# Kernel optimization log

Hardware: AMD Instinct MI355X
Metric: run time of the kernel (lower is better)

Reference implementation:

```python
import jax, jax.numpy as jnp
from jax import lax
import numpy as np

IN, HID, NCLS, B, S = 360, 64, 5, 64, 128
MH_CONST = 2.0 / (np.sqrt(3.0) * np.pi ** 0.25)


def setup_inputs() -> dict:
    key = jax.random.key(0)
    ks = jax.random.split(key, 24)
    g = lambda i, shape, s=0.05: jax.random.normal(ks[i], shape, jnp.float32) * s
    inp = {
        'x_seq': jax.random.normal(ks[0], (B, S, IN), jnp.float32),
        # WavKANLinear params (out=64, in=360)
        'wav_scale': jnp.ones((HID, IN), jnp.float32),
        'wav_translation': jnp.zeros((HID, IN), jnp.float32),
        'wav_weights': g(1, (HID, IN)),
        'base_weight': g(2, (HID, IN)),
        # BatchNorm1d (eval mode, running stats)
        'bn_gamma': jnp.ones((HID,), jnp.float32),
        'bn_beta': jnp.zeros((HID,), jnp.float32),
        'bn_mean': jnp.zeros((HID,), jnp.float32),
        'bn_var': jnp.ones((HID,), jnp.float32),
        # LayerNorm(64)
        'ln_gamma': jnp.ones((HID,), jnp.float32),
        'ln_beta': jnp.zeros((HID,), jnp.float32),
        # bidirectional GRU, 1 layer, hidden=64
        'gru_w_ih_f': g(3, (3 * HID, HID)), 'gru_w_hh_f': g(4, (3 * HID, HID)),
        'gru_b_ih_f': g(5, (3 * HID,)), 'gru_b_hh_f': g(6, (3 * HID,)),
        'gru_w_ih_b': g(7, (3 * HID, HID)), 'gru_w_hh_b': g(8, (3 * HID, HID)),
        'gru_b_ih_b': g(9, (3 * HID,)), 'gru_b_hh_b': g(10, (3 * HID,)),
        # classifier: Linear(128,64) -> ReLU -> Linear(64,5)
        'fc1_w': g(11, (HID, 2 * HID)), 'fc1_b': jnp.zeros((HID,), jnp.float32),
        'fc2_w': g(12, (NCLS, HID)), 'fc2_b': jnp.zeros((NCLS,), jnp.float32),
    }
    return inp


def _gru_dir(x_sbf, w_ih, w_hh, b_ih, b_hh, reverse):
    # x_sbf: (S, B, F). Returns final hidden (B, H). PyTorch GRU equations.
    Bn = x_sbf.shape[1]
    H = w_hh.shape[1]
    gi_all = jnp.einsum('sbf,gf->sbg', x_sbf, w_ih) + b_ih  # precompute input gates

    def step(h, gi):
        gh = h @ w_hh.T + b_hh
        i_r, i_z, i_n = jnp.split(gi, 3, axis=-1)
        h_r, h_z, h_n = jnp.split(gh, 3, axis=-1)
        r = jax.nn.sigmoid(i_r + h_r)
        z = jax.nn.sigmoid(i_z + h_z)
        n = jnp.tanh(i_n + r * h_n)
        h_new = (1.0 - z) * n + z * h
        return h_new, None

    h0 = jnp.zeros((Bn, H), x_sbf.dtype)
    h_final, _ = lax.scan(step, h0, gi_all, reverse=reverse)
    return h_final


def reference(x_seq, wav_scale, wav_translation, wav_weights, base_weight,
              bn_gamma, bn_beta, bn_mean, bn_var, ln_gamma, ln_beta,
              gru_w_ih_f, gru_w_hh_f, gru_b_ih_f, gru_b_hh_f,
              gru_w_ih_b, gru_w_hh_b, gru_b_ih_b, gru_b_hh_b,
              fc1_w, fc1_b, fc2_w, fc2_b):
    b, s, f = x_seq.shape
    x_flat = x_seq.reshape(b * s, f)  # (N, 360)

    # --- WavKANLinear (mexican_hat) ---
    x_scaled = (x_flat[:, None, :] - wav_translation[None]) / wav_scale[None]  # (N, 64, 360)
    wavelet = MH_CONST * (x_scaled * x_scaled - 1.0) * jnp.exp(-0.5 * x_scaled * x_scaled)
    wav_out = jnp.einsum('noi,oi->no', wavelet, wav_weights)  # (N, 64)
    base_out = jax.nn.silu(x_flat) @ base_weight.T
    combined = wav_out + base_out
    # BatchNorm1d eval mode
    x_emb = (combined - bn_mean) * lax.rsqrt(bn_var + 1e-5) * bn_gamma + bn_beta

    # --- LayerNorm(64) ---
    mu = jnp.mean(x_emb, axis=-1, keepdims=True)
    var = jnp.mean(jnp.square(x_emb - mu), axis=-1, keepdims=True)
    x_emb = (x_emb - mu) * lax.rsqrt(var + 1e-5) * ln_gamma + ln_beta
    # dropout is identity in eval mode

    x_sbf = x_emb.reshape(b, s, HID).swapaxes(0, 1)  # (S, B, 64)

    # --- bidirectional GRU, take final hiddens ---
    h_fwd = _gru_dir(x_sbf, gru_w_ih_f, gru_w_hh_f, gru_b_ih_f, gru_b_hh_f, False)
    h_bwd = _gru_dir(x_sbf, gru_w_ih_b, gru_w_hh_b, gru_b_ih_b, gru_b_hh_b, True)
    hidden_cat = jnp.concatenate([h_fwd, h_bwd], axis=1)  # (B, 128)

    # --- classifier ---
    h = jax.nn.relu(hidden_cat @ fc1_w.T + fc1_b)
    logits = h @ fc2_w.T + fc2_b
    return logits
```

## Files before the change

kernel.cpp:

```cpp
#include <hip/hip_runtime.h>

#define IN_F   360
#define HIDN   64
#define NCLS   5
#define BATCH  64
#define SEQ    128
#define NROWS  (BATCH*SEQ)

#define WS_FLAG  0
#define WS_WPACK 16
#define WS_WFAST 92176
#define WS_WT4   138256
#define WS_XEMB  162832
#define WS_GI    687120
#define WS_HC    3832848

#define LOG2E        1.4426950408889634f
#define NEG_HALF_L2E (-0.7213475204444817f)

__device__ __forceinline__ float fast_rcp(float x) { return __builtin_amdgcn_rcpf(x); }
__device__ __forceinline__ float fast_rsq(float x) { return __builtin_amdgcn_rsqf(x); }
__device__ __forceinline__ float sigmoid_(float x) {
    x = fminf(fmaxf(x, -60.0f), 60.0f);
    return fast_rcp(1.0f + exp2f(-LOG2E * x));
}
__device__ __forceinline__ float tanh_(float x) {
    x = fminf(fmaxf(x, -30.0f), 30.0f);
    float e = exp2f(-2.8853900817779268f * x);
    return (1.0f - e) * fast_rcp(1.0f + e);
}
__device__ __forceinline__ float readlane_f(float v, int l) {
    return __int_as_float(__builtin_amdgcn_readlane(__float_as_int(v), l));
}

__global__ __launch_bounds__(256) void prep_kernel(
    const float* __restrict__ scale, const float* __restrict__ trans,
    const float* __restrict__ ww,    const float* __restrict__ bw,
    const float* __restrict__ wihf,  const float* __restrict__ wihb,
    float* __restrict__ ws) {
    int idx = blockIdx.x * 256 + threadIdx.x;
    float4* wpack  = (float4*)(ws + WS_WPACK);
    float2* wfast2 = (float2*)(ws + WS_WFAST);
    float*  wT4    = ws + WS_WT4;
    int*    flagp  = (int*)(ws + WS_FLAG);
    if (idx < 64 * IN_F) {
        int o = idx & 63, i = idx >> 6;
        float s  = scale[o * IN_F + i];
        float tr = trans[o * IN_F + i];
        if (s != 1.0f || tr != 0.0f) atomicOr(flagp, 1);
        float a  = 1.0f / s;
        float b  = -tr * a;
        float wq = 0.8673250705840776f * ww[o * IN_F + i];
        float bb = bw[o * IN_F + i];
        wpack[i * 64 + o] = make_float4(a, b, wq, bb);
        wfast2[(i >> 1) * 128 + o * 2 + (i & 1)] = make_float2(wq, bb);
    }
    int idx2 = idx - 64 * IN_F;
    if (idx2 >= 0 && idx2 < 24576) {
        int e = idx2 & 3; int rest = idx2 >> 2;
        int g = rest % 384; int k4 = rest / 384;
        int k = k4 * 4 + e; int dir = g / 192; int gg = g - dir * 192;
        const float* src = dir ? wihb : wihf;
        wT4[idx2] = src[gg * 64 + k];
    }
}

__global__ __launch_bounds__(256) void wavkan_kernel(
    const float* __restrict__ x_seq,
    const float* __restrict__ bn_g, const float* __restrict__ bn_b,
    const float* __restrict__ bn_m, const float* __restrict__ bn_v,
    const float* __restrict__ ln_g, const float* __restrict__ ln_b,
    const float* __restrict__ ws_c, float* __restrict__ x_emb) {
    __shared__ float2 xs_lds[16 * IN_F];
    int t = threadIdx.x;
    int row0 = blockIdx.x * 16;
    int o = t & 63, grp = t >> 6;
    int fast = (*(const int*)(ws_c + WS_FLAG)) == 0;

    float acc0 = 0.f, acc1 = 0.f, acc2 = 0.f, acc3 = 0.f;

    if (fast) {
        for (int idx = t; idx < 16 * IN_F; idx += 256) {
            int r = idx / IN_F, i = idx - r * IN_F;
            float x = x_seq[(row0 + r) * IN_F + i];
            float u = x * x;
            float phi = (u - 1.0f) * exp2f(u * NEG_HALF_L2E);
            float sl  = x * fast_rcp(1.0f + exp2f(-LOG2E * x));
            xs_lds[idx] = make_float2(phi, sl);
        }
        __syncthreads();
        const float4* wf4 = (const float4*)(ws_c + WS_WFAST);
        const float4* xs4 = (const float4*)xs_lds;
        const float4* xr0 = xs4 + (grp * 4 + 0) * 180;
        const float4* xr1 = xs4 + (grp * 4 + 1) * 180;
        const float4* xr2 = xs4 + (grp * 4 + 2) * 180;
        const float4* xr3 = xs4 + (grp * 4 + 3) * 180;
        #pragma unroll 2
        for (int i2 = 0; i2 < 180; ++i2) {
            float4 wp = wf4[i2 * 64 + o];
            float4 a = xr0[i2];
            acc0 = fmaf(a.x, wp.x, acc0); acc0 = fmaf(a.y, wp.y, acc0);
            acc0 = fmaf(a.z, wp.z, acc0); acc0 = fmaf(a.w, wp.w, acc0);
            float4 b = xr1[i2];
            acc1 = fmaf(b.x, wp.x, acc1); acc1 = fmaf(b.y, wp.y, acc1);
            acc1 = fmaf(b.z, wp.z, acc1); acc1 = fmaf(b.w, wp.w, acc1);
            float4 c = xr2[i2];
            acc2 = fmaf(c.x, wp.x, acc2); acc2 = fmaf(c.y, wp.y, acc2);
            acc2 = fmaf(c.z, wp.z, acc2); acc2 = fmaf(c.w, wp.w, acc2);
            float4 d = xr3[i2];
            acc3 = fmaf(d.x, wp.x, acc3); acc3 = fmaf(d.y, wp.y, acc3);
            acc3 = fmaf(d.z, wp.z, acc3); acc3 = fmaf(d.w, wp.w, acc3);
        }
    } else {
        for (int idx = t; idx < 16 * IN_F; idx += 256) {
            int r = idx / IN_F, i = idx - r * IN_F;
            float x = x_seq[(row0 + r) * IN_F + i];
            float sl = x * fast_rcp(1.0f + exp2f(-LOG2E * x));
            xs_lds[idx] = make_float2(x, sl);
        }
        __syncthreads();
        const float4* wpack = (const float4*)(ws_c + WS_WPACK);
        const float2* xr0 = xs_lds + (grp * 4 + 0) * IN_F;
        const float2* xr1 = xs_lds + (grp * 4 + 1) * IN_F;
        const float2* xr2 = xs_lds + (grp * 4 + 2) * IN_F;
        const float2* xr3 = xs_lds + (grp * 4 + 3) * IN_F;
        for (int i = 0; i < IN_F; ++i) {
            float4 wp = wpack[i * 64 + o];
            {
                float2 xs = xr0[i];
                float xsc = fmaf(xs.x, wp.x, wp.y); float u = xsc * xsc;
                float e = exp2f(u * NEG_HALF_L2E);
                acc0 = fmaf((u - 1.0f) * e, wp.z, acc0);
                acc0 = fmaf(xs.y, wp.w, acc0);
            }
            {
                float2 xs = xr1[i];
                float xsc = fmaf(xs.x, wp.x, wp.y); float u = xsc * xsc;
                float e = exp2f(u * NEG_HALF_L2E);
                acc1 = fmaf((u - 1.0f) * e, wp.z, acc1);
                acc1 = fmaf(xs.y, wp.w, acc1);
            }
            {
                float2 xs = xr2[i];
                float xsc = fmaf(xs.x, wp.x, wp.y); float u = xsc * xsc;
                float e = exp2f(u * NEG_HALF_L2E);
                acc2 = fmaf((u - 1.0f) * e, wp.z, acc2);
                acc2 = fmaf(xs.y, wp.w, acc2);
            }
            {
                float2 xs = xr3[i];
                float xsc = fmaf(xs.x, wp.x, wp.y); float u = xsc * xsc;
                float e = exp2f(u * NEG_HALF_L2E);
                acc3 = fmaf((u - 1.0f) * e, wp.z, acc3);
                acc3 = fmaf(xs.y, wp.w, acc3);
            }
        }
    }

    float bscale = bn_g[o] * fast_rsq(bn_v[o] + 1e-5f);
    float bshift = fmaf(-bn_m[o], bscale, bn_b[o]);
    float lg = ln_g[o], lb = ln_b[o];
    float vals[4] = {acc0, acc1, acc2, acc3};
    #pragma unroll
    for (int rr = 0; rr < 4; ++rr) {
        float y = fmaf(vals[rr], bscale, bshift);
        float s = y;
        #pragma unroll
        for (int m = 1; m < 64; m <<= 1) s += __shfl_xor(s, m, 64);
        float mu = s * (1.0f / 64.0f);
        float d = y - mu;
        float s2 = d * d;
        #pragma unroll
        for (int m = 1; m < 64; m <<= 1) s2 += __shfl_xor(s2, m, 64);
        float rstd = fast_rsq(s2 * (1.0f / 64.0f) + 1e-5f);
        x_emb[(row0 + grp * 4 + rr) * 64 + o] = fmaf(d * rstd, lg, lb);
    }
}

__global__ __launch_bounds__(384) void gi_kernel(
    const float* __restrict__ ws_c,
    const float* __restrict__ bihf, const float* __restrict__ bihb,
    float* __restrict__ gi) {
    __shared__ __align__(16) float xs[32 * 64];
    const float4* wT4   = (const float4*)(ws_c + WS_WT4);
    const float*  x_emb = ws_c + WS_XEMB;
    int t = threadIdx.x;
    int row0 = blockIdx.x * 32;
    {
        const float4* src = (const float4*)(x_emb + row0 * 64);
        float4* dst = (float4*)xs;
        for (int i = t; i < 512; i += 384) dst[i] = src[i];
    }
    int dir = t / 192, gg = t - dir * 192;
    float bih = dir ? bihb[gg] : bihf[gg];
    float4 w[16];
    #pragma unroll
    for (int k4 = 0; k4 < 16; ++k4) w[k4] = wT4[k4 * 384 + t];
    __syncthreads();
    for (int r = 0; r < 32; r += 2) {
        const float4* x0 = (const float4*)(xs + r * 64);
        const float4* x1 = (const float4*)(xs + r * 64 + 64);
        float a0 = bih, a1 = 0.f, b0 = bih, b1 = 0.f;
        #pragma unroll
        for (int k4 = 0; k4 < 16; k4 += 2) {
            float4 xv = x0[k4];     float4 wv = w[k4];
            a0 = fmaf(xv.x, wv.x, a0); a0 = fmaf(xv.y, wv.y, a0);
            a0 = fmaf(xv.z, wv.z, a0); a0 = fmaf(xv.w, wv.w, a0);
            float4 xu = x0[k4 + 1]; float4 wu = w[k4 + 1];
            a1 = fmaf(xu.x, wu.x, a1); a1 = fmaf(xu.y, wu.y, a1);
            a1 = fmaf(xu.z, wu.z, a1); a1 = fmaf(xu.w, wu.w, a1);
            float4 yv = x1[k4];
            b0 = fmaf(yv.x, wv.x, b0); b0 = fmaf(yv.y, wv.y, b0);
            b0 = fmaf(yv.z, wv.z, b0); b0 = fmaf(yv.w, wv.w, b0);
            float4 yu = x1[k4 + 1];
            b1 = fmaf(yu.x, wu.x, b1); b1 = fmaf(yu.y, wu.y, b1);
            b1 = fmaf(yu.z, wu.z, b1); b1 = fmaf(yu.w, wu.w, b1);
        }
        gi[(row0 + r) * 384 + t]     = a0 + a1;
        gi[(row0 + r + 1) * 384 + t] = b0 + b1;
    }
}

__global__ __launch_bounds__(192, 1) void gru_kernel(
    const float* __restrict__ ws_c,
    const float* __restrict__ whhf, const float* __restrict__ bhhf,
    const float* __restrict__ whhb, const float* __restrict__ bhhb,
    float* __restrict__ hc) {
    __shared__ __align__(16) float gi_l[64 * 192];
    __shared__ float gh[2][192];
    const float* gi = ws_c + WS_GI;
    int t = threadIdx.x, lane = t & 63;
    int b = blockIdx.x & 63, dir = blockIdx.x >> 6;
    const float* whh = dir ? whhb : whhf;
    const float* bhh = dir ? bhhb : bhhf;

    float w[64];
    {
        const float4* wrow = (const float4*)(whh + t * 64);
        #pragma unroll
        for (int q = 0; q < 16; ++q) {
            float4 a = wrow[q];
            w[4*q] = a.x; w[4*q+1] = a.y; w[4*q+2] = a.z; w[4*q+3] = a.w;
        }
    }
    float bias = bhh[t];

    const float* gsrc = gi + (size_t)(b * SEQ) * 384 + dir * 192 + t;
    #pragma unroll
    for (int q = 0; q < 64; ++q) {
        int sidx = dir ? (SEQ - 1 - q) : q;
        gi_l[q * 192 + t] = gsrc[sidx * 384];
    }
    float pf[64];
    #pragma unroll
    for (int q = 0; q < 64; ++q) {
        int sidx = dir ? (SEQ - 1 - (64 + q)) : (64 + q);
        pf[q] = gsrc[sidx * 384];
    }
    float hreg = 0.0f;
    __syncthreads();

    for (int ss = 0; ss < SEQ; ++ss) {
        if (ss == 64) {
            __syncthreads();
            #pragma unroll
            for (int q = 0; q < 64; ++q) gi_l[q * 192 + t] = pf[q];
            __syncthreads();
        }
        int ssl = ss & 63;
        float a0 = bias, a1 = 0.f, a2 = 0.f, a3 = 0.f;
        #pragma unroll
        for (int k = 0; k < 64; k += 4) {
            float h0 = readlane_f(hreg, k);
            float h1 = readlane_f(hreg, k + 1);
            float h2 = readlane_f(hreg, k + 2);
            float h3 = readlane_f(hreg, k + 3);
            a0 = fmaf(w[k],     h0, a0);
            a1 = fmaf(w[k + 1], h1, a1);
            a2 = fmaf(w[k + 2], h2, a2);
            a3 = fmaf(w[k + 3], h3, a3);
        }
        int p = ss & 1;
        gh[p][t] = (a0 + a1) + (a2 + a3);
        float ir  = gi_l[ssl * 192 + lane];
        float iz  = gi_l[ssl * 192 + 64 + lane];
        float in_ = gi_l[ssl * 192 + 128 + lane];
        __syncthreads();
        float r = sigmoid_(ir + gh[p][lane]);
        float z = sigmoid_(iz + gh[p][64 + lane]);
        float n = tanh_(fmaf(r, gh[p][128 + lane], in_));
        hreg = fmaf(z, hreg - n, n);
    }
    if (t < 64) hc[b * 128 + dir * 64 + lane] = hreg;
}

__global__ __launch_bounds__(64) void head_kernel(
    const float* __restrict__ ws_c,
    const float* __restrict__ fc1w, const float* __restrict__ fc1b,
    const float* __restrict__ fc2w, const float* __restrict__ fc2b,
    float* __restrict__ out) {
    __shared__ __align__(16) float hr[128];
    __shared__ float h1[64];
    const float* hc = ws_c + WS_HC;
    int bb = blockIdx.x, t = threadIdx.x;
    hr[t]      = hc[bb * 128 + t];
    hr[64 + t] = hc[bb * 128 + 64 + t];
    __syncthreads();
    float acc = fc1b[t];
    const float4* w4 = (const float4*)(fc1w + t * 128);
    const float4* h4 = (const float4*)hr;
    #pragma unroll 8
    for (int k4 = 0; k4 < 32; ++k4) {
        float4 wv = w4[k4]; float4 hv = h4[k4];
        acc = fmaf(hv.x, wv.x, acc); acc = fmaf(hv.y, wv.y, acc);
        acc = fmaf(hv.z, wv.z, acc); acc = fmaf(hv.w, wv.w, acc);
    }
    h1[t] = fmaxf(acc, 0.0f);
    __syncthreads();
    if (t < NCLS) {
        float acc2 = fc2b[t];
        const float* wr = fc2w + t * 64;
        #pragma unroll 8
        for (int k = 0; k < 64; ++k) acc2 = fmaf(h1[k], wr[k], acc2);
        out[bb * NCLS + t] = acc2;
    }
}

extern "C" void kernel_launch(void* const* d_in, const int* in_sizes, int n_in,
                              void* d_out, int out_size, void* d_ws, size_t ws_size,
                              hipStream_t stream) {
    const float* x_seq = (const float*)d_in[0];
    const float* wscal = (const float*)d_in[1];
    const float* wtran = (const float*)d_in[2];
    const float* wwght = (const float*)d_in[3];
    const float* bwght = (const float*)d_in[4];
    const float* bn_g  = (const float*)d_in[5];
    const float* bn_b  = (const float*)d_in[6];
    const float* bn_m  = (const float*)d_in[7];
    const float* bn_v  = (const float*)d_in[8];
    const float* ln_g  = (const float*)d_in[9];
    const float* ln_b  = (const float*)d_in[10];
    const float* wihf  = (const float*)d_in[11];
    const float* whhf  = (const float*)d_in[12];
    const float* bihf  = (const float*)d_in[13];
    const float* bhhf  = (const float*)d_in[14];
    const float* wihb  = (const float*)d_in[15];
    const float* whhb  = (const float*)d_in[16];
    const float* bihb  = (const float*)d_in[17];
    const float* bhhb  = (const float*)d_in[18];
    const float* fc1w  = (const float*)d_in[19];
    const float* fc1b  = (const float*)d_in[20];
    const float* fc2w  = (const float*)d_in[21];
    const float* fc2b  = (const float*)d_in[22];
    float* ws  = (float*)d_ws;
    float* out = (float*)d_out;

    hipMemsetAsync(ws + WS_FLAG, 0, sizeof(int), stream);
    hipLaunchKernelGGL(prep_kernel, dim3(186), dim3(256), 0, stream,
                       wscal, wtran, wwght, bwght, wihf, wihb, ws);
    hipLaunchKernelGGL(wavkan_kernel, dim3(NROWS / 16), dim3(256), 0, stream,
                       x_seq, bn_g, bn_b, bn_m, bn_v, ln_g, ln_b, ws, ws + WS_XEMB);
    hipLaunchKernelGGL(gi_kernel, dim3(NROWS / 32), dim3(384), 0, stream,
                       ws, bihf, bihb, ws + WS_GI);
    hipLaunchKernelGGL(gru_kernel, dim3(128), dim3(192), 0, stream,
                       ws, whhf, bhhf, whhb, bhhb, ws + WS_HC);
    hipLaunchKernelGGL(head_kernel, dim3(64), dim3(64), 0, stream,
                       ws, fc1w, fc1b, fc2w, fc2b, out);
}
```

Before: 226.6 us.

## Run GRU recurrence in a single wavefront computing all three gates per lane

The GRU kernel now uses one 64-lane wavefront per (batch, direction), with each lane holding the r, z and n rows of W_hh in registers. This removes the per-step block barrier and the LDS exchange of hidden-gate results. Input gate values are loaded directly from global memory two steps ahead instead of being staged in LDS. The trade-off is three times the FMA work per lane and much higher register usage, and the global loads of the gate inputs may not be fully hidden.

```diff
diff --git a/kernel.cpp b/kernel.cpp
--- a/kernel.cpp
+++ b/kernel.cpp
@@ -221,77 +221,81 @@
     }
 }
 
-__global__ __launch_bounds__(192, 1) void gru_kernel(
+__global__ __launch_bounds__(64, 1) void gru_kernel(
     const float* __restrict__ ws_c,
     const float* __restrict__ whhf, const float* __restrict__ bhhf,
     const float* __restrict__ whhb, const float* __restrict__ bhhb,
     float* __restrict__ hc) {
-    __shared__ __align__(16) float gi_l[64 * 192];
-    __shared__ float gh[2][192];
     const float* gi = ws_c + WS_GI;
-    int t = threadIdx.x, lane = t & 63;
+    int t = threadIdx.x;
     int b = blockIdx.x & 63, dir = blockIdx.x >> 6;
     const float* whh = dir ? whhb : whhf;
     const float* bhh = dir ? bhhb : bhhf;
 
-    float w[64];
+    float wr[64], wz[64], wn[64];
     {
-        const float4* wrow = (const float4*)(whh + t * 64);
+        const float4* r4 = (const float4*)(whh + t * 64);
+        const float4* z4 = (const float4*)(whh + (64 + t) * 64);
+        const float4* n4 = (const float4*)(whh + (128 + t) * 64);
         #pragma unroll
         for (int q = 0; q < 16; ++q) {
-            float4 a = wrow[q];
-            w[4*q] = a.x; w[4*q+1] = a.y; w[4*q+2] = a.z; w[4*q+3] = a.w;
-        }
-    }
-    float bias = bhh[t];
-
-    const float* gsrc = gi + (size_t)(b * SEQ) * 384 + dir * 192 + t;
-    #pragma unroll
-    for (int q = 0; q < 64; ++q) {
-        int sidx = dir ? (SEQ - 1 - q) : q;
-        gi_l[q * 192 + t] = gsrc[sidx * 384];
-    }
-    float pf[64];
-    #pragma unroll
-    for (int q = 0; q < 64; ++q) {
-        int sidx = dir ? (SEQ - 1 - (64 + q)) : (64 + q);
-        pf[q] = gsrc[sidx * 384];
-    }
-    float hreg = 0.0f;
-    __syncthreads();
-
-    for (int ss = 0; ss < SEQ; ++ss) {
-        if (ss == 64) {
-            __syncthreads();
+            float4 a = r4[q];
+            wr[4*q] = a.x; wr[4*q+1] = a.y; wr[4*q+2] = a.z; wr[4*q+3] = a.w;
+            float4 c = z4[q];
+            wz[4*q] = c.x; wz[4*q+1] = c.y; wz[4*q+2] = c.z; wz[4*q+3] = c.w;
+            float4 d = n4[q];
+            wn[4*q] = d.x; wn[4*q+1] = d.y; wn[4*q+2] = d.z; wn[4*q+3] = d.w;
+        }
+    }
+    float br = bhh[t], bz = bhh[64 + t], bn = bhh[128 + t];
+
+    const float* g = gi + (size_t)(b * SEQ) * 384 + dir * 192 + t;
+#define GOFF(s) ((dir ? (SEQ - 1 - (s)) : (s)) * 384)
+    float ar0, az0, an0, ar1, az1, an1;
+    { const float* p = g + GOFF(0); ar0 = p[0]; az0 = p[64]; an0 = p[128]; }
+    { const float* p = g + GOFF(1); ar1 = p[0]; az1 = p[64]; an1 = p[128]; }
+    float h = 0.0f;
+
+    for (int s = 0; s < SEQ; s += 2) {
+        {
+            float a_r = br, a_z = bz, a_n = bn;
             #pragma unroll
-            for (int q = 0; q < 64; ++q) gi_l[q * 192 + t] = pf[q];
-            __syncthreads();
-        }
-        int ssl = ss & 63;
-        float a0 = bias, a1 = 0.f, a2 = 0.f, a3 = 0.f;
-        #pragma unroll
-        for (int k = 0; k < 64; k += 4) {
-            float h0 = readlane_f(hreg, k);
-            float h1 = readlane_f(hreg, k + 1);
-            float h2 = readlane_f(hreg, k + 2);
-            float h3 = readlane_f(hreg, k + 3);
-            a0 = fmaf(w[k],     h0, a0);
-            a1 = fmaf(w[k + 1], h1, a1);
-            a2 = fmaf(w[k + 2], h2, a2);
-            a3 = fmaf(w[k + 3], h3, a3);
-        }
-        int p = ss & 1;
-        gh[p][t] = (a0 + a1) + (a2 + a3);
-        float ir  = gi_l[ssl * 192 + lane];
-        float iz  = gi_l[ssl * 192 + 64 + lane];
-        float in_ = gi_l[ssl * 192 + 128 + lane];
-        __syncthreads();
-        float r = sigmoid_(ir + gh[p][lane]);
-        float z = sigmoid_(iz + gh[p][64 + lane]);
-        float n = tanh_(fmaf(r, gh[p][128 + lane], in_));
-        hreg = fmaf(z, hreg - n, n);
-    }
-    if (t < 64) hc[b * 128 + dir * 64 + lane] = hreg;
+            for (int k = 0; k < 64; ++k) {
+                float hk = readlane_f(h, k);
+                a_r = fmaf(wr[k], hk, a_r);
+                a_z = fmaf(wz[k], hk, a_z);
+                a_n = fmaf(wn[k], hk, a_n);
+            }
+            float r = sigmoid_(ar0 + a_r);
+            float z = sigmoid_(az0 + a_z);
+            float n = tanh_(fmaf(r, a_n, an0));
+            h = fmaf(z, h - n, n);
+        }
+        if (s + 2 < SEQ) {
+            const float* p = g + GOFF(s + 2);
+            ar0 = p[0]; az0 = p[64]; an0 = p[128];
+        }
+        {
+            float a_r = br, a_z = bz, a_n = bn;
+            #pragma unroll
+            for (int k = 0; k < 64; ++k) {
+                float hk = readlane_f(h, k);
+                a_r = fmaf(wr[k], hk, a_r);
+                a_z = fmaf(wz[k], hk, a_z);
+                a_n = fmaf(wn[k], hk, a_n);
+            }
+            float r = sigmoid_(ar1 + a_r);
+            float z = sigmoid_(az1 + a_z);
+            float n = tanh_(fmaf(r, a_n, an1));
+            h = fmaf(z, h - n, n);
+        }
+        if (s + 3 < SEQ) {
+            const float* p = g + GOFF(s + 3);
+            ar1 = p[0]; az1 = p[64]; an1 = p[128];
+        }
+    }
+#undef GOFF
+    hc[b * 128 + dir * 64 + t] = h;
 }
 
 __global__ __launch_bounds__(64) void head_kernel(
@@ -362,7 +366,7 @@
                        x_seq, bn_g, bn_b, bn_m, bn_v, ln_g, ln_b, ws, ws + WS_XEMB);
     hipLaunchKernelGGL(gi_kernel, dim3(NROWS / 32), dim3(384), 0, stream,
                        ws, bihf, bihb, ws + WS_GI);
-    hipLaunchKernelGGL(gru_kernel, dim3(128), dim3(192), 0, stream,
+    hipLaunchKernelGGL(gru_kernel, dim3(128), dim3(64), 0, stream,
                        ws, whhf, bhhf, whhb, bhhb, ws + WS_HC);
     hipLaunchKernelGGL(head_kernel, dim3(64), dim3(64), 0, stream,
                        ws, fc1w, fc1b, fc2w, fc2b, out);
```

Measured after the change: 246.8 us. +8.9%, slower.
